# Performance work log

Measured on AMD Instinct MI355X. Metric: run time of the kernel, lower is better.

The kernel has to match this reference:

```python
import jax, jax.numpy as jnp
import numpy as np

B, T, C, K = 1024, 500, 64, 2000  # batch, timesteps, latent chains (KCs), observed KCs
S, O = 2, 2                       # n_states, n_outputs (hard-coded in BktModel)


def setup_inputs() -> dict:
    key = jax.random.key(0)
    k1, k2, k3, k4, k5, k6 = jax.random.split(key, 6)
    corr = jax.random.randint(k1, (B, T), 0, O)
    kc = jax.random.randint(k2, (B, T), 0, K)
    # soft KC-membership matrix (stands in for gumbel_softmax sample; rows sum to 1)
    A = jax.nn.softmax(jax.random.normal(k3, (K, C)), axis=1)
    trans_logits = jax.random.normal(k4, (C, S, S))
    obs_logits = jax.random.normal(k5, (C, S, O))
    init_logits = jax.random.normal(k6, (C, S))
    return dict(corr=corr, kc=kc, A=A, trans_logits=trans_logits,
                obs_logits=obs_logits, init_logits=init_logits)


def _hmm_forward(obs, chain, trans_logits, obs_logits, init_logits):
    # obs: [B,T] int, chain: [B,T,C] float
    n_batch = obs.shape[0]
    log_obs = jax.nn.log_softmax(obs_logits, axis=2)   # [C,S,O]
    log_t = jax.nn.log_softmax(trans_logits, axis=1)   # [C,S,S] (normalized over dim 1, as in torch)
    log_alpha0 = jnp.tile(jax.nn.log_softmax(init_logits, axis=1)[None], (n_batch, 1, 1))  # [B,C,S]

    def step(log_alpha, xs):
        y, cc = xs  # y: [B] int, cc: [B,C]
        # predictive distribution over outputs
        a1 = jnp.einsum('bc,cso->bso', cc, log_obs)          # [B,S,O]
        a2 = jnp.einsum('bc,bcs->bs', cc, log_alpha)         # [B,S]
        log_py = jax.scipy.special.logsumexp(a1 + a2[:, :, None], axis=1)  # [B,O]
        log_py = jax.nn.log_softmax(log_py, axis=1)
        # state update for the active chains
        lo_y = jnp.transpose(log_obs[:, :, y], (2, 0, 1))    # [B,C,S]
        lp = jnp.einsum('bcs,bc->bs', lo_y, cc)              # [B,S]
        a1c = jnp.einsum('bcs,bc->bs', log_alpha, cc)        # [B,S]
        a2c = jnp.einsum('bc,cst->bst', cc, log_t)           # [B,S,S]
        a3 = jax.scipy.special.logsumexp(lp[:, None, :] + a1c[:, None, :] + a2c, axis=2)  # [B,S]
        new_la = (1.0 - cc)[:, :, None] * log_alpha + cc[:, :, None] * a3[:, None, :]
        return new_la, log_py

    _, outs = jax.lax.scan(step, log_alpha0,
                           (obs.T, jnp.transpose(chain, (1, 0, 2))))
    return jnp.transpose(outs, (1, 0, 2))  # [B,T,O]


def reference(corr, kc, A, trans_logits, obs_logits, init_logits):
    chain = A[kc]  # [B,T,C]
    return _hmm_forward(corr, chain, trans_logits, obs_logits, init_logits)
```

## Files before the change

kernel.cpp:

```cpp
#include <hip/hip_runtime.h>
#include <math.h>

#define BB 1024
#define TT 500
#define CC_ 64
#define KK 2000

#define LOG2E 1.44269504088896340736f
#define LN2   0.69314718055994530942f

#if __has_builtin(__builtin_amdgcn_exp2f)
__device__ __forceinline__ float fast_exp2(float x) { return __builtin_amdgcn_exp2f(x); }
#else
__device__ __forceinline__ float fast_exp2(float x) { return exp2f(x); }
#endif
#if __has_builtin(__builtin_amdgcn_logf)
__device__ __forceinline__ float fast_log2(float x) { return __builtin_amdgcn_logf(x); }
#else
__device__ __forceinline__ float fast_log2(float x) { return log2f(x); }
#endif

__device__ __forceinline__ float lse2_2(float a, float b) {
    float m = fmaxf(a, b);
    float d = fminf(a, b) - m;
    return m + fast_log2(1.0f + fast_exp2(d));
}

template<int CTRL, int RM, int BM>
__device__ __forceinline__ float dpp_add(float x) {
    int s = __builtin_amdgcn_update_dpp(0, __float_as_int(x), CTRL, RM, BM, true);
    return x + __int_as_float(s);
}
__device__ __forceinline__ float wave_sum63(float x) {
    x = dpp_add<0x111, 0xf, 0xf>(x);
    x = dpp_add<0x112, 0xf, 0xf>(x);
    x = dpp_add<0x114, 0xf, 0xf>(x);
    x = dpp_add<0x118, 0xf, 0xf>(x);
    x = dpp_add<0x142, 0xa, 0xf>(x);
    x = dpp_add<0x143, 0xc, 0xf>(x);
    return x;
}
__device__ __forceinline__ float bcast63(float x) {
    return __int_as_float(__builtin_amdgcn_readlane(__float_as_int(x), 63));
}

__global__ __launch_bounds__(64) void precompute_P(
    const float* __restrict__ A,
    const float* __restrict__ trans_logits,
    const float* __restrict__ obs_logits,
    float* __restrict__ P)
{
    int k = blockIdx.x;
    int c = threadIdx.x;

    float ob[2][2];
#pragma unroll
    for (int s = 0; s < 2; ++s) {
        float o0 = obs_logits[c * 4 + s * 2 + 0] * LOG2E;
        float o1 = obs_logits[c * 4 + s * 2 + 1] * LOG2E;
        float l = lse2_2(o0, o1);
        ob[s][0] = o0 - l;
        ob[s][1] = o1 - l;
    }
    float lt[2][2];
    {
        float t00 = trans_logits[c * 4 + 0] * LOG2E;
        float t01 = trans_logits[c * 4 + 1] * LOG2E;
        float t10 = trans_logits[c * 4 + 2] * LOG2E;
        float t11 = trans_logits[c * 4 + 3] * LOG2E;
        float l0 = lse2_2(t00, t10);
        float l1 = lse2_2(t01, t11);
        lt[0][0] = t00 - l0; lt[0][1] = t01 - l1;
        lt[1][0] = t10 - l0; lt[1][1] = t11 - l1;
    }

    float a = A[k * CC_ + c];
    float v[8];
    v[0] = a * ob[0][0]; v[1] = a * ob[0][1];
    v[2] = a * ob[1][0]; v[3] = a * ob[1][1];
    v[4] = a * lt[0][0]; v[5] = a * lt[0][1];
    v[6] = a * lt[1][0]; v[7] = a * lt[1][1];

#pragma unroll
    for (int i = 0; i < 8; ++i) v[i] = wave_sum63(v[i]);
    if (c == 63) {
#pragma unroll
        for (int i = 0; i < 8; ++i) P[k * 8 + i] = v[i];
    }
}

__global__ __launch_bounds__(64) void bkt_main(
    const int* __restrict__ corr,
    const int* __restrict__ kc,
    const float* __restrict__ A,
    const float* __restrict__ init_logits,
    const float* __restrict__ P,
    float* __restrict__ out)
{
    int b = blockIdx.x;
    int c = threadIdx.x;

    int z;
    asm("v_mov_b32 %0, 0" : "=v"(z));

    float la0, la1;
    {
        float i0 = init_logits[c * 2 + 0] * LOG2E;
        float i1 = init_logits[c * 2 + 1] * LOG2E;
        float l = lse2_2(i0, i1);
        la0 = i0 - l;
        la1 = i1 - l;
    }

    const int* kcb = kc + b * TT;
    const int* cb  = corr + b * TT;
    float2* outb   = (float2*)(out + (size_t)b * TT * 2);

    int kq[8], yq[8];
#pragma unroll
    for (int i = 0; i < 8; ++i) {
        kq[i] = kcb[i + z];
        yq[i] = cb[i + z];
    }
    float  ccq[4];
    float4 paq[4], pbq[4];
#pragma unroll
    for (int i = 0; i < 3; ++i) {
        ccq[i] = A[kq[i] * CC_ + c];
        paq[i] = *(const float4*)(P + kq[i] * 8);
        pbq[i] = *(const float4*)(P + kq[i] * 8 + 4);
    }

    for (int tt = 0; tt < 504; tt += 8) {
#pragma unroll
        for (int j = 0; j < 8; ++j) {
            int t = tt + j;
            int t8 = t + 8; if (t8 > TT - 1) t8 = TT - 1;
            int knew = kcb[t8 + z];
            int ynew = cb[t8 + z];
            int kp = kq[(j + 3) & 7];
            ccq[(j + 3) & 3] = A[kp * CC_ + c];
            paq[(j + 3) & 3] = *(const float4*)(P + kp * 8);
            pbq[(j + 3) & 3] = *(const float4*)(P + kp * 8 + 4);
            int y = yq[j];
            kq[j] = knew;
            yq[j] = ynew;
            float cc   = ccq[j & 3];
            float4 a1v = paq[j & 3];
            float4 qv  = pbq[j & 3];

            float x0 = wave_sum63(cc * la0);
            float x1 = wave_sum63(cc * la1);
            if (t < TT && c == 63) outb[t] = make_float2(x0, x1);
            float r0 = bcast63(x0);
            float r1 = bcast63(x1);

            float w0 = (y == 0 ? a1v.x : a1v.y) + r0;
            float w1 = (y == 0 ? a1v.z : a1v.w) + r1;
            float a30 = fast_log2(fast_exp2(w0 + qv.x) + fast_exp2(w1 + qv.y));
            float a31 = fast_log2(fast_exp2(w0 + qv.z) + fast_exp2(w1 + qv.w));
            la0 = la0 + cc * (a30 - la0) - r0;
            la1 = la1 + cc * (a31 - la1) - r0;
        }
    }
}

__global__ __launch_bounds__(256) void finish_py(
    const int* __restrict__ kc,
    const float* __restrict__ P,
    float* __restrict__ out)
{
    int i = blockIdx.x * 256 + threadIdx.x;
    if (i >= BB * TT) return;
    int k = kc[i];
    float2 r = ((const float2*)out)[i];
    float4 pa = *(const float4*)(P + k * 8);
    float lo0 = lse2_2(pa.x + r.x, pa.z + r.y);
    float lo1 = lse2_2(pa.y + r.x, pa.w + r.y);
    float lz  = lse2_2(lo0, lo1);
    ((float2*)out)[i] = make_float2((lo0 - lz) * LN2, (lo1 - lz) * LN2);
}

extern "C" void kernel_launch(void* const* d_in, const int* in_sizes, int n_in,
                              void* d_out, int out_size, void* d_ws, size_t ws_size,
                              hipStream_t stream) {
    const int* corr    = (const int*)d_in[0];
    const int* kc      = (const int*)d_in[1];
    const float* A     = (const float*)d_in[2];
    const float* trans = (const float*)d_in[3];
    const float* obs   = (const float*)d_in[4];
    const float* init  = (const float*)d_in[5];
    float* out = (float*)d_out;

    float* P = (float*)d_ws;

    precompute_P<<<KK, 64, 0, stream>>>(A, trans, obs, P);
    bkt_main<<<BB, 64, 0, stream>>>(corr, kc, A, init, P, out);
    finish_py<<<(BB * TT + 255) / 256, 256, 0, stream>>>(kc, P, out);
}
```

Baseline: 102.7 us.

## Pack four batch rows per wave with 16 lanes each and precombine transition tables

The main recurrence now gives each batch row 16 lanes, each holding 4 chains, so one 64-lane wave processes four batch rows. The full-wave reduction plus readlane broadcast is replaced by a 16-lane row DPP reduction. The per-KC table is split into an observation table and a y-indexed table with pre-exponentiated terms, which removes one exp per state per step and the y select. The aim is to cut reduction latency and per-step transcendental work, at the cost of launching 4x fewer workgroups (256 waves) and doing more per-lane FMAs.

```diff
diff --git a/kernel.cpp b/kernel.cpp
--- a/kernel.cpp
+++ b/kernel.cpp
@@ -40,15 +40,20 @@
     x = dpp_add<0x143, 0xc, 0xf>(x);
     return x;
 }
-__device__ __forceinline__ float bcast63(float x) {
-    return __int_as_float(__builtin_amdgcn_readlane(__float_as_int(x), 63));
+__device__ __forceinline__ float rowsum16(float x) {
+    x = dpp_add<0x121, 0xf, 0xf>(x);
+    x = dpp_add<0x122, 0xf, 0xf>(x);
+    x = dpp_add<0x124, 0xf, 0xf>(x);
+    x = dpp_add<0x128, 0xf, 0xf>(x);
+    return x;
 }
 
 __global__ __launch_bounds__(64) void precompute_P(
     const float* __restrict__ A,
     const float* __restrict__ trans_logits,
     const float* __restrict__ obs_logits,
-    float* __restrict__ P)
+    float* __restrict__ PA,
+    float* __restrict__ P3)
 {
     int k = blockIdx.x;
     int c = threadIdx.x;
@@ -84,8 +89,17 @@
 #pragma unroll
     for (int i = 0; i < 8; ++i) v[i] = wave_sum63(v[i]);
     if (c == 63) {
-#pragma unroll
-        for (int i = 0; i < 8; ++i) P[k * 8 + i] = v[i];
+        ((float4*)PA)[k] = make_float4(v[0], v[1], v[2], v[3]);
+#pragma unroll
+        for (int y = 0; y < 2; ++y) {
+            float sel0 = v[y];
+            float sel1 = v[2 + y];
+            ((float4*)P3)[k * 2 + y] = make_float4(
+                fast_exp2(sel0 + v[4]),
+                fast_exp2(sel0 + v[6]),
+                sel1 + v[5],
+                sel1 + v[7]);
+        }
     }
 }
 
@@ -94,22 +108,21 @@
     const int* __restrict__ kc,
     const float* __restrict__ A,
     const float* __restrict__ init_logits,
-    const float* __restrict__ P,
+    const float* __restrict__ P3,
     float* __restrict__ out)
 {
-    int b = blockIdx.x;
-    int c = threadIdx.x;
-
-    int z;
-    asm("v_mov_b32 %0, 0" : "=v"(z));
-
-    float la0, la1;
-    {
-        float i0 = init_logits[c * 2 + 0] * LOG2E;
-        float i1 = init_logits[c * 2 + 1] * LOG2E;
+    int lane = threadIdx.x;
+    int g = lane >> 4, i = lane & 15;
+    int b = blockIdx.x * 4 + g;
+
+    float la[4][2];
+#pragma unroll
+    for (int j = 0; j < 4; ++j) {
+        float i0 = init_logits[(4 * i + j) * 2 + 0] * LOG2E;
+        float i1 = init_logits[(4 * i + j) * 2 + 1] * LOG2E;
         float l = lse2_2(i0, i1);
-        la0 = i0 - l;
-        la1 = i1 - l;
+        la[j][0] = i0 - l;
+        la[j][1] = i1 - l;
     }
 
     const int* kcb = kc + b * TT;
@@ -118,67 +131,74 @@
 
     int kq[8], yq[8];
 #pragma unroll
-    for (int i = 0; i < 8; ++i) {
-        kq[i] = kcb[i + z];
-        yq[i] = cb[i + z];
-    }
-    float  ccq[4];
-    float4 paq[4], pbq[4];
-#pragma unroll
-    for (int i = 0; i < 3; ++i) {
-        ccq[i] = A[kq[i] * CC_ + c];
-        paq[i] = *(const float4*)(P + kq[i] * 8);
-        pbq[i] = *(const float4*)(P + kq[i] * 8 + 4);
-    }
-
-    for (int tt = 0; tt < 504; tt += 8) {
+    for (int q = 0; q < 8; ++q) { kq[q] = kcb[q]; yq[q] = cb[q]; }
+
+    float4 ccq[4], pq[4];
+#pragma unroll
+    for (int q = 0; q < 3; ++q) {
+        ccq[q] = *(const float4*)(A + kq[q] * CC_ + 4 * i);
+        pq[q]  = ((const float4*)P3)[kq[q] * 2 + yq[q]];
+    }
+
+    for (int tt = 0; tt <= 496; tt += 8) {
 #pragma unroll
         for (int j = 0; j < 8; ++j) {
             int t = tt + j;
             int t8 = t + 8; if (t8 > TT - 1) t8 = TT - 1;
-            int knew = kcb[t8 + z];
-            int ynew = cb[t8 + z];
-            int kp = kq[(j + 3) & 7];
-            ccq[(j + 3) & 3] = A[kp * CC_ + c];
-            paq[(j + 3) & 3] = *(const float4*)(P + kp * 8);
-            pbq[(j + 3) & 3] = *(const float4*)(P + kp * 8 + 4);
-            int y = yq[j];
-            kq[j] = knew;
-            yq[j] = ynew;
-            float cc   = ccq[j & 3];
-            float4 a1v = paq[j & 3];
-            float4 qv  = pbq[j & 3];
-
-            float x0 = wave_sum63(cc * la0);
-            float x1 = wave_sum63(cc * la1);
-            if (t < TT && c == 63) outb[t] = make_float2(x0, x1);
-            float r0 = bcast63(x0);
-            float r1 = bcast63(x1);
-
-            float w0 = (y == 0 ? a1v.x : a1v.y) + r0;
-            float w1 = (y == 0 ? a1v.z : a1v.w) + r1;
-            float a30 = fast_log2(fast_exp2(w0 + qv.x) + fast_exp2(w1 + qv.y));
-            float a31 = fast_log2(fast_exp2(w0 + qv.z) + fast_exp2(w1 + qv.w));
-            la0 = la0 + cc * (a30 - la0) - r0;
-            la1 = la1 + cc * (a31 - la1) - r0;
+            int knew = kcb[t8];
+            int ynew = cb[t8];
+            int kp = kq[(j + 3) & 7], yp = yq[(j + 3) & 7];
+            ccq[(j + 3) & 3] = *(const float4*)(A + kp * CC_ + 4 * i);
+            pq[(j + 3) & 3]  = ((const float4*)P3)[kp * 2 + yp];
+
+            float4 cc = ccq[j & 3];
+            float4 pr = pq[j & 3];
+            kq[j] = knew; yq[j] = ynew;
+
+            float x0 = (cc.x * la[0][0] + cc.y * la[1][0])
+                     + (cc.z * la[2][0] + cc.w * la[3][0]);
+            float x1 = (cc.x * la[0][1] + cc.y * la[1][1])
+                     + (cc.z * la[2][1] + cc.w * la[3][1]);
+            x0 = rowsum16(x0);
+            x1 = rowsum16(x1);
+            if (t < TT && i == 0) outb[t] = make_float2(x0, x1);
+
+            float d   = x1 - x0;
+            float a30 = fast_log2(pr.x + fast_exp2(pr.z + d));
+            float a31 = fast_log2(pr.y + fast_exp2(pr.w + d));
+            {
+                float g0, g1;
+                g0 = la[0][0] - x0; g1 = la[0][1] - x0;
+                la[0][0] = g0 + cc.x * (a30 - g0);
+                la[0][1] = g1 + cc.x * (a31 - g1);
+                g0 = la[1][0] - x0; g1 = la[1][1] - x0;
+                la[1][0] = g0 + cc.y * (a30 - g0);
+                la[1][1] = g1 + cc.y * (a31 - g1);
+                g0 = la[2][0] - x0; g1 = la[2][1] - x0;
+                la[2][0] = g0 + cc.z * (a30 - g0);
+                la[2][1] = g1 + cc.z * (a31 - g1);
+                g0 = la[3][0] - x0; g1 = la[3][1] - x0;
+                la[3][0] = g0 + cc.w * (a30 - g0);
+                la[3][1] = g1 + cc.w * (a31 - g1);
+            }
         }
     }
 }
 
 __global__ __launch_bounds__(256) void finish_py(
     const int* __restrict__ kc,
-    const float* __restrict__ P,
+    const float* __restrict__ PA,
     float* __restrict__ out)
 {
-    int i = blockIdx.x * 256 + threadIdx.x;
-    if (i >= BB * TT) return;
-    int k = kc[i];
-    float2 r = ((const float2*)out)[i];
-    float4 pa = *(const float4*)(P + k * 8);
+    int idx = blockIdx.x * 256 + threadIdx.x;
+    if (idx >= BB * TT) return;
+    int k = kc[idx];
+    float2 r  = ((const float2*)out)[idx];
+    float4 pa = ((const float4*)PA)[k];
     float lo0 = lse2_2(pa.x + r.x, pa.z + r.y);
     float lo1 = lse2_2(pa.y + r.x, pa.w + r.y);
     float lz  = lse2_2(lo0, lo1);
-    ((float2*)out)[i] = make_float2((lo0 - lz) * LN2, (lo1 - lz) * LN2);
+    ((float2*)out)[idx] = make_float2((lo0 - lz) * LN2, (lo1 - lz) * LN2);
 }
 
 extern "C" void kernel_launch(void* const* d_in, const int* in_sizes, int n_in,
@@ -192,9 +212,10 @@
     const float* init  = (const float*)d_in[5];
     float* out = (float*)d_out;
 
-    float* P = (float*)d_ws;
-
-    precompute_P<<<KK, 64, 0, stream>>>(A, trans, obs, P);
-    bkt_main<<<BB, 64, 0, stream>>>(corr, kc, A, init, P, out);
-    finish_py<<<(BB * TT + 255) / 256, 256, 0, stream>>>(kc, P, out);
-}
+    float* PA = (float*)d_ws;
+    float* P3 = PA + KK * 4;
+
+    precompute_P<<<KK, 64, 0, stream>>>(A, trans, obs, PA, P3);
+    bkt_main<<<BB / 4, 64, 0, stream>>>(corr, kc, A, init, P3, out);
+    finish_py<<<(BB * TT + 255) / 256, 256, 0, stream>>>(kc, PA, out);
+}
```

After: 94.55 us. -7.9%, faster.
